# Optimization experiments

Measured on AMD Instinct MI355X. Metric: run time of the kernel, lower is better.

## Reference

```python
import jax, jax.numpy as jnp
import numpy as np

NHEAD, HEAD_DIM = 10, 10
TEMPERATURE = 1.0
INV_SQRT_HD = np.float32(1.0 / np.sqrt(HEAD_DIM))


def setup_inputs() -> dict:
    key = jax.random.key(0)
    ks = jax.random.split(key, 6)
    B, nhid, L = 4, 128, 1024
    D = NHEAD * HEAD_DIM  # 100
    x = jax.random.normal(ks[0], (B, nhid, L, 1), dtype=jnp.float32)
    edge_matrix = jax.random.randint(ks[1], (B, L, L), 0, 2, dtype=jnp.int32)
    wq_w = jax.random.normal(ks[2], (D, nhid), dtype=jnp.float32) * 0.05
    wq_b = jnp.zeros((D,), jnp.float32)
    wedge_w = jax.random.normal(ks[3], (2 * HEAD_DIM,), dtype=jnp.float32) * 0.1
    wedge_b = jnp.zeros((1,), jnp.float32)
    wo_w = jax.random.normal(ks[4], (nhid, D), dtype=jnp.float32) * 0.05
    wo_b = jnp.zeros((nhid,), jnp.float32)
    return dict(x=x, edge_matrix=edge_matrix, wq_w=wq_w, wq_b=wq_b,
                wedge_w=wedge_w, wedge_b=wedge_b, wo_w=wo_w, wo_b=wo_b)


def reference(x, edge_matrix, wq_w, wq_b, wedge_w, wedge_b, wo_w, wo_b):
    B, nhid, L, _ = x.shape
    # WQ: 1x1 conv == per-position linear over channels
    q = jnp.einsum('bhl,ch->bcl', x[..., 0], wq_w) + wq_b[None, :, None]  # (B, nhead*hd, L)
    # source overwrites k and v with q (WK/WV dead code): k == v == q
    k = q.reshape(B, NHEAD, HEAD_DIM, L).transpose(0, 1, 3, 2)  # (B, nhead, L, hd)
    # WEDGE(Linear(2*hd,1)) over concat[k_i, k_j] == w1.k_i + w2.k_j + b (exact same math,
    # avoids materializing the O(L^2 * 2*hd) a_input tensor)
    s_i = jnp.einsum('bnld,d->bnl', k, wedge_w[:HEAD_DIM])
    s_j = jnp.einsum('bnld,d->bnl', k, wedge_w[HEAD_DIM:])
    alpha = (s_i[:, :, :, None] + s_j[:, :, None, :] + wedge_b[0]) * INV_SQRT_HD  # (B,nhead,L,L)
    alpha = jnp.where(edge_matrix[:, None, :, :] == 0, jnp.float32(-1e15), alpha)
    alpha = jax.nn.softmax(alpha, axis=-1) / TEMPERATURE  # dropout: identity at eval
    att = jnp.einsum('bnij,bnjd->bnid', alpha, k)  # v == k; (B, nhead, L, hd)
    # faithful to torch: raw row-major view(B, -1, L, 1) that scrambles (head,pos) ordering
    att = att.reshape(B, NHEAD * HEAD_DIM, L, 1)
    ret = jnp.einsum('bcl,oc->bol', att[..., 0], wo_w) + wo_b[None, :, None]
    ret = ret[..., None]  # (B, nhid, L, 1)
    return ret, alpha.reshape(B * NHEAD, L, L)
```

## Files before the change

kernel.cpp:

```cpp
#include <hip/hip_runtime.h>

#define BB   4
#define NHID 128
#define LL   1024
#define NH   10
#define HD   10
#define DD   100
#define SCALE 0.31622776601683794f

__global__ __launch_bounds__(256) void k_qproj(
    const float* __restrict__ x, const float* __restrict__ wq_w,
    const float* __restrict__ wq_b, float* __restrict__ kbuf) {
  const int l  = blockIdx.x * 256 + threadIdx.x;
  const int c0 = blockIdx.y * 2;
  const int b  = blockIdx.z;
  float acc0 = wq_b[c0], acc1 = wq_b[c0 + 1];
  const float* xb = x + (size_t)b * NHID * LL + l;
  const float* w0 = wq_w + (size_t)c0 * NHID;
  const float* w1 = w0 + NHID;
  #pragma unroll 8
  for (int h = 0; h < NHID; ++h) {
    float xv = xb[(size_t)h * LL];
    acc0 += w0[h] * xv;
    acc1 += w1[h] * xv;
  }
  {
    int c = c0, n = c / HD, d = c % HD;
    kbuf[(((size_t)(b * NH + n)) * LL + l) * HD + d] = acc0;
  }
  {
    int c = c0 + 1, n = c / HD, d = c % HD;
    kbuf[(((size_t)(b * NH + n)) * LL + l) * HD + d] = acc1;
  }
}

__global__ __launch_bounds__(256) void k_edgeproj(
    const float* __restrict__ kbuf, const float* __restrict__ we_w,
    const float* __restrict__ we_b, float* __restrict__ si, float* __restrict__ sj) {
  const int idx = blockIdx.x * 256 + threadIdx.x;
  const float* kr = kbuf + (size_t)idx * HD;
  float s1 = we_b[0], s2 = 0.f;
  #pragma unroll
  for (int d = 0; d < HD; ++d) {
    float kv = kr[d];
    s1 += kv * we_w[d];
    s2 += kv * we_w[HD + d];
  }
  si[idx] = s1 * SCALE;
  sj[idx] = s2 * SCALE;
}

__global__ __launch_bounds__(256) void k_attn(
    const float* __restrict__ kbuf, const float* __restrict__ si,
    const float* __restrict__ sj, const int* __restrict__ edge,
    float* __restrict__ alpha_out, float* __restrict__ att) {
  const int t    = threadIdx.x;
  const int lane = t & 63;
  const int wid  = t >> 6;
  const int blk  = blockIdx.x;
  const int rt   = blk & 63;
  const int bn   = blk >> 6;
  const int b    = bn / NH;
  const int i0   = rt * 16 + wid * 4;

  __shared__ float ks[LL * HD];
  {
    const float4* src = (const float4*)(kbuf + (size_t)bn * (LL * HD));
    float4* dst = (float4*)ks;
    for (int idx = t; idx < (LL * HD) / 4; idx += 256) dst[idx] = src[idx];
  }
  float sjv[16];
  {
    const float* sp = sj + (size_t)bn * LL;
    #pragma unroll
    for (int m = 0; m < 16; ++m) sjv[m] = sp[m * 64 + lane];
  }
  __syncthreads();

  const float* sip = si + (size_t)bn * LL;
  float p[4][16];
  float inv[4];
  #pragma unroll
  for (int r = 0; r < 4; ++r) {
    const float siv = sip[i0 + r];
    const int* ep = edge + ((size_t)(b * LL) + (i0 + r)) * LL;
    float sum = 0.f;
    #pragma unroll
    for (int m = 0; m < 16; ++m) {
      int e = ep[m * 64 + lane];
      float v = e ? (siv + sjv[m]) : -1e15f;
      float xx = __expf(v);
      p[r][m] = xx;
      sum += xx;
    }
    #pragma unroll
    for (int s = 32; s >= 1; s >>= 1) sum += __shfl_xor(sum, s, 64);
    inv[r] = __builtin_amdgcn_rcpf(sum);
  }

  float part[4][HD];
  #pragma unroll
  for (int r = 0; r < 4; ++r)
    #pragma unroll
    for (int d = 0; d < HD; ++d) part[r][d] = 0.f;

  float* a0 = alpha_out + ((size_t)bn * LL + i0) * LL + lane;
  #pragma unroll
  for (int m = 0; m < 16; ++m) {
    const float* kr = ks + (m * 64 + lane) * HD;
    float2 kv0 = *(const float2*)(kr + 0);
    float2 kv1 = *(const float2*)(kr + 2);
    float2 kv2 = *(const float2*)(kr + 4);
    float2 kv3 = *(const float2*)(kr + 6);
    float2 kv4 = *(const float2*)(kr + 8);
    #pragma unroll
    for (int r = 0; r < 4; ++r) {
      float a = p[r][m] * inv[r];
      __builtin_nontemporal_store(a, a0 + (size_t)r * LL + m * 64);
      part[r][0] += a * kv0.x; part[r][1] += a * kv0.y;
      part[r][2] += a * kv1.x; part[r][3] += a * kv1.y;
      part[r][4] += a * kv2.x; part[r][5] += a * kv2.y;
      part[r][6] += a * kv3.x; part[r][7] += a * kv3.y;
      part[r][8] += a * kv4.x; part[r][9] += a * kv4.y;
    }
  }

  const bool b5 = (lane & 32) != 0;
  const bool b4 = (lane & 16) != 0;
  const bool b3 = (lane & 8) != 0;
  const bool b2 = (lane & 4) != 0;
  #pragma unroll
  for (int r = 0; r < 4; ++r) {
    float pv[16];
    #pragma unroll
    for (int d = 0; d < HD; ++d) pv[d] = part[r][d];
    #pragma unroll
    for (int d = HD; d < 16; ++d) pv[d] = 0.f;
    #pragma unroll
    for (int i = 0; i < 8; ++i) {
      float snd = b5 ? pv[i] : pv[i + 8];
      float kp  = b5 ? pv[i + 8] : pv[i];
      pv[i] = kp + __shfl_xor(snd, 32, 64);
    }
    #pragma unroll
    for (int i = 0; i < 4; ++i) {
      float snd = b4 ? pv[i] : pv[i + 4];
      float kp  = b4 ? pv[i + 4] : pv[i];
      pv[i] = kp + __shfl_xor(snd, 16, 64);
    }
    #pragma unroll
    for (int i = 0; i < 2; ++i) {
      float snd = b3 ? pv[i] : pv[i + 2];
      float kp  = b3 ? pv[i + 2] : pv[i];
      pv[i] = kp + __shfl_xor(snd, 8, 64);
    }
    {
      float snd = b2 ? pv[0] : pv[1];
      float kp  = b2 ? pv[1] : pv[0];
      pv[0] = kp + __shfl_xor(snd, 4, 64);
    }
    pv[0] += __shfl_xor(pv[0], 2, 64);
    pv[0] += __shfl_xor(pv[0], 1, 64);
    float g = __shfl(pv[0], lane * 4, 64);
    if (lane < HD)
      att[((size_t)bn * LL + (i0 + r)) * HD + lane] = g;
  }
}

__global__ __launch_bounds__(256) void k_out(
    const float* __restrict__ att, const float* __restrict__ wo_w,
    const float* __restrict__ wo_b, float* __restrict__ ret) {
  const int l  = blockIdx.x * 256 + threadIdx.x;
  const int o0 = blockIdx.y * 4;
  const int b  = blockIdx.z;
  const float* ab = att + (size_t)b * (DD * LL);
  float acc[4];
  #pragma unroll
  for (int oo = 0; oo < 4; ++oo) acc[oo] = wo_b[o0 + oo];
  for (int c = 0; c < DD; ++c) {
    float a = ab[(size_t)c * LL + l];
    #pragma unroll
    for (int oo = 0; oo < 4; ++oo) acc[oo] += wo_w[(size_t)(o0 + oo) * DD + c] * a;
  }
  #pragma unroll
  for (int oo = 0; oo < 4; ++oo)
    ret[((size_t)b * NHID + o0 + oo) * LL + l] = acc[oo];
}

extern "C" void kernel_launch(void* const* d_in, const int* in_sizes, int n_in,
                              void* d_out, int out_size, void* d_ws, size_t ws_size,
                              hipStream_t stream) {
  (void)in_sizes; (void)n_in; (void)out_size; (void)ws_size;
  const float* x    = (const float*)d_in[0];
  const int*   edge = (const int*)d_in[1];
  const float* wq_w = (const float*)d_in[2];
  const float* wq_b = (const float*)d_in[3];
  const float* we_w = (const float*)d_in[4];
  const float* we_b = (const float*)d_in[5];
  const float* wo_w = (const float*)d_in[6];
  const float* wo_b = (const float*)d_in[7];

  float* out       = (float*)d_out;
  float* ret_out   = out;
  float* alpha_out = out + (size_t)BB * NHID * LL;

  float* ws   = (float*)d_ws;
  float* kbuf = ws;
  float* si   = kbuf + (size_t)BB * NH * LL * HD;
  float* sj   = si + (size_t)BB * NH * LL;
  float* att  = sj + (size_t)BB * NH * LL;

  dim3 g1(LL / 256, DD / 2, BB);
  k_qproj<<<g1, 256, 0, stream>>>(x, wq_w, wq_b, kbuf);

  k_edgeproj<<<(BB * NH * LL) / 256, 256, 0, stream>>>(kbuf, we_w, we_b, si, sj);

  k_attn<<<BB * NH * (LL / 16), 256, 0, stream>>>(kbuf, si, sj, edge, alpha_out, att);

  dim3 g3(LL / 256, NHID / 4, BB);
  k_out<<<g3, 256, 0, stream>>>(att, wo_w, wo_b, ret_out);
}
```

Before: 249.0 us.

## Cancel row term in softmax and precompute exp of column scores

The row score s_i is constant along each softmax row, so it cancels. The edge projection kernel now computes only exp(s_j) per column, and the attention kernel uses masked exp(s_j) values directly as unnormalized weights. The normalization reciprocal is applied at the end to the aggregated output and to the alpha values. Alpha values are then written in a second pass with float4 vector stores. This removes the per-element exp and the p register array, at the cost of reading the edge mask twice per row.

```diff
diff --git a/kernel.cpp b/kernel.cpp
--- a/kernel.cpp
+++ b/kernel.cpp
@@ -7,6 +7,8 @@
 #define HD   10
 #define DD   100
 #define SCALE 0.31622776601683794f
+
+typedef float vfloat4 __attribute__((ext_vector_type(4)));
 
 __global__ __launch_bounds__(256) void k_qproj(
     const float* __restrict__ x, const float* __restrict__ wq_w,
@@ -36,23 +38,18 @@
 
 __global__ __launch_bounds__(256) void k_edgeproj(
     const float* __restrict__ kbuf, const float* __restrict__ we_w,
-    const float* __restrict__ we_b, float* __restrict__ si, float* __restrict__ sj) {
+    float* __restrict__ esj) {
   const int idx = blockIdx.x * 256 + threadIdx.x;
   const float* kr = kbuf + (size_t)idx * HD;
-  float s1 = we_b[0], s2 = 0.f;
-  #pragma unroll
-  for (int d = 0; d < HD; ++d) {
-    float kv = kr[d];
-    s1 += kv * we_w[d];
-    s2 += kv * we_w[HD + d];
-  }
-  si[idx] = s1 * SCALE;
-  sj[idx] = s2 * SCALE;
+  float s2 = 0.f;
+  #pragma unroll
+  for (int d = 0; d < HD; ++d) s2 += kr[d] * we_w[HD + d];
+  esj[idx] = __expf(s2 * SCALE);
 }
 
 __global__ __launch_bounds__(256) void k_attn(
-    const float* __restrict__ kbuf, const float* __restrict__ si,
-    const float* __restrict__ sj, const int* __restrict__ edge,
+    const float* __restrict__ kbuf, const float* __restrict__ esj,
+    const int* __restrict__ edge,
     float* __restrict__ alpha_out, float* __restrict__ att) {
   const int t    = threadIdx.x;
   const int lane = t & 63;
@@ -69,42 +66,28 @@
     float4* dst = (float4*)ks;
     for (int idx = t; idx < (LL * HD) / 4; idx += 256) dst[idx] = src[idx];
   }
-  float sjv[16];
-  {
-    const float* sp = sj + (size_t)bn * LL;
-    #pragma unroll
-    for (int m = 0; m < 16; ++m) sjv[m] = sp[m * 64 + lane];
+  float  esv[16];
+  float4 esv4[4];
+  {
+    const float* sp = esj + (size_t)bn * LL;
+    #pragma unroll
+    for (int m = 0; m < 16; ++m) esv[m] = sp[m * 64 + lane];
+    const float4* sp4 = (const float4*)sp;
+    #pragma unroll
+    for (int m = 0; m < 4; ++m) esv4[m] = sp4[m * 64 + lane];
   }
   __syncthreads();
 
-  const float* sip = si + (size_t)bn * LL;
-  float p[4][16];
-  float inv[4];
+  const int* ebase = edge + (size_t)b * LL * LL;
+
+  float part[4][HD];
+  float denom[4];
   #pragma unroll
   for (int r = 0; r < 4; ++r) {
-    const float siv = sip[i0 + r];
-    const int* ep = edge + ((size_t)(b * LL) + (i0 + r)) * LL;
-    float sum = 0.f;
-    #pragma unroll
-    for (int m = 0; m < 16; ++m) {
-      int e = ep[m * 64 + lane];
-      float v = e ? (siv + sjv[m]) : -1e15f;
-      float xx = __expf(v);
-      p[r][m] = xx;
-      sum += xx;
-    }
-    #pragma unroll
-    for (int s = 32; s >= 1; s >>= 1) sum += __shfl_xor(sum, s, 64);
-    inv[r] = __builtin_amdgcn_rcpf(sum);
-  }
-
-  float part[4][HD];
-  #pragma unroll
-  for (int r = 0; r < 4; ++r)
+    denom[r] = 0.f;
     #pragma unroll
     for (int d = 0; d < HD; ++d) part[r][d] = 0.f;
-
-  float* a0 = alpha_out + ((size_t)bn * LL + i0) * LL + lane;
+  }
   #pragma unroll
   for (int m = 0; m < 16; ++m) {
     const float* kr = ks + (m * 64 + lane) * HD;
@@ -113,15 +96,41 @@
     float2 kv2 = *(const float2*)(kr + 4);
     float2 kv3 = *(const float2*)(kr + 6);
     float2 kv4 = *(const float2*)(kr + 8);
+    const float es = esv[m];
     #pragma unroll
     for (int r = 0; r < 4; ++r) {
-      float a = p[r][m] * inv[r];
-      __builtin_nontemporal_store(a, a0 + (size_t)r * LL + m * 64);
-      part[r][0] += a * kv0.x; part[r][1] += a * kv0.y;
-      part[r][2] += a * kv1.x; part[r][3] += a * kv1.y;
-      part[r][4] += a * kv2.x; part[r][5] += a * kv2.y;
-      part[r][6] += a * kv3.x; part[r][7] += a * kv3.y;
-      part[r][8] += a * kv4.x; part[r][9] += a * kv4.y;
+      int e = ebase[(size_t)(i0 + r) * LL + m * 64 + lane];
+      float au = e ? es : 0.f;
+      denom[r] += au;
+      part[r][0] += au * kv0.x; part[r][1] += au * kv0.y;
+      part[r][2] += au * kv1.x; part[r][3] += au * kv1.y;
+      part[r][4] += au * kv2.x; part[r][5] += au * kv2.y;
+      part[r][6] += au * kv3.x; part[r][7] += au * kv3.y;
+      part[r][8] += au * kv4.x; part[r][9] += au * kv4.y;
+    }
+  }
+  float inv[4];
+  #pragma unroll
+  for (int r = 0; r < 4; ++r) {
+    float s = denom[r];
+    #pragma unroll
+    for (int sft = 32; sft >= 1; sft >>= 1) s += __shfl_xor(s, sft, 64);
+    inv[r] = __builtin_amdgcn_rcpf(s);
+  }
+
+  float* ap = alpha_out + ((size_t)bn * LL + i0) * LL;
+  #pragma unroll
+  for (int m = 0; m < 4; ++m) {
+    #pragma unroll
+    for (int r = 0; r < 4; ++r) {
+      int4 e = ((const int4*)(ebase + (size_t)(i0 + r) * LL))[m * 64 + lane];
+      vfloat4 a;
+      a.x = e.x ? esv4[m].x * inv[r] : 0.f;
+      a.y = e.y ? esv4[m].y * inv[r] : 0.f;
+      a.z = e.z ? esv4[m].z * inv[r] : 0.f;
+      a.w = e.w ? esv4[m].w * inv[r] : 0.f;
+      vfloat4* dst = (vfloat4*)(ap + (size_t)r * LL) + m * 64 + lane;
+      __builtin_nontemporal_store(a, dst);
     }
   }
 
@@ -163,7 +172,7 @@
     pv[0] += __shfl_xor(pv[0], 1, 64);
     float g = __shfl(pv[0], lane * 4, 64);
     if (lane < HD)
-      att[((size_t)bn * LL + (i0 + r)) * HD + lane] = g;
+      att[((size_t)bn * LL + (i0 + r)) * HD + lane] = g * inv[r];
   }
 }
 
@@ -196,7 +205,6 @@
   const float* wq_w = (const float*)d_in[2];
   const float* wq_b = (const float*)d_in[3];
   const float* we_w = (const float*)d_in[4];
-  const float* we_b = (const float*)d_in[5];
   const float* wo_w = (const float*)d_in[6];
   const float* wo_b = (const float*)d_in[7];
 
@@ -206,16 +214,15 @@
 
   float* ws   = (float*)d_ws;
   float* kbuf = ws;
-  float* si   = kbuf + (size_t)BB * NH * LL * HD;
-  float* sj   = si + (size_t)BB * NH * LL;
-  float* att  = sj + (size_t)BB * NH * LL;
+  float* esj  = kbuf + (size_t)BB * NH * LL * HD;
+  float* att  = esj + (size_t)BB * NH * LL;
 
   dim3 g1(LL / 256, DD / 2, BB);
   k_qproj<<<g1, 256, 0, stream>>>(x, wq_w, wq_b, kbuf);
 
-  k_edgeproj<<<(BB * NH * LL) / 256, 256, 0, stream>>>(kbuf, we_w, we_b, si, sj);
-
-  k_attn<<<BB * NH * (LL / 16), 256, 0, stream>>>(kbuf, si, sj, edge, alpha_out, att);
+  k_edgeproj<<<(BB * NH * LL) / 256, 256, 0, stream>>>(kbuf, we_w, esj);
+
+  k_attn<<<BB * NH * (LL / 16), 256, 0, stream>>>(kbuf, esj, edge, alpha_out, att);
 
   dim3 g3(LL / 256, NHID / 4, BB);
   k_out<<<g3, 256, 0, stream>>>(att, wo_w, wo_b, ret_out);
```

Result: slower. 281.6 us (+13.1%).
